# Kernel tuning notes

Measured on AMD Instinct MI355X. Metric: run time of the kernel, lower is better.

The kernel has to match this reference:

```python
import jax, jax.numpy as jnp
import numpy as np

B, T, F, U, O = 256, 1024, 37, 64, 1


def setup_inputs() -> dict:
    key = jax.random.key(0)
    ks = jax.random.split(key, 8)
    return {
        "demo": jax.random.normal(ks[0], (B, 8), dtype=jnp.float32),
        "times": jax.random.uniform(ks[1], (B, T), dtype=jnp.float32),
        "values": jax.random.normal(ks[2], (B, T, F), dtype=jnp.float32),
        "measurements": jax.random.uniform(ks[3], (B, T, F), dtype=jnp.float32),
        "lengths": jax.random.randint(ks[4], (B,), 1, T + 1),
        # Keras GRU params (reset_after=True): kernel [F,3U], recurrent_kernel [U,3U], bias [2,3U]
        "kernel": jax.random.normal(ks[5], (F, 3 * U), dtype=jnp.float32) * 0.05,
        "recurrent_kernel": jax.random.normal(ks[6], (U, 3 * U), dtype=jnp.float32) * 0.05,
        "bias": jnp.zeros((2, 3 * U), dtype=jnp.float32),
        "dense_w": jax.random.normal(ks[7], (U, O), dtype=jnp.float32) * 0.05,
        "dense_b": jnp.zeros((O,), dtype=jnp.float32),
    }


def _gru_model(values, lengths, kernel, recurrent_kernel, bias, dense_w, dense_b, seq_len):
    # tf.sequence_mask(lengths, maxlen=T)
    mask = jnp.arange(seq_len)[None, :] < lengths[:, None]  # [B, T] bool
    # input projection hoisted out of the recurrence: [B, T, 3U]
    x_proj = values @ kernel + bias[0]

    n_units = recurrent_kernel.shape[0]

    def step(h, inp):
        xp, m = inp                       # xp: [B, 3U], m: [B]
        hp = h @ recurrent_kernel + bias[1]
        xz, xr, xh = jnp.split(xp, 3, axis=-1)
        hz, hr, hh = jnp.split(hp, 3, axis=-1)
        z = jax.nn.sigmoid(xz + hz)
        r = jax.nn.sigmoid(xr + hr)
        cand = jnp.tanh(xh + r * hh)      # reset_after=True: reset applied after recurrent matmul
        h_new = z * h + (1.0 - z) * cand
        # Keras masking: masked steps keep previous state/output
        h = jnp.where(m[:, None], h_new, h)
        return h, h

    h0 = jnp.zeros((values.shape[0], n_units), values.dtype)
    _, hs = jax.lax.scan(step, h0, (jnp.swapaxes(x_proj, 0, 1), jnp.swapaxes(mask, 0, 1)))
    gru_out = jnp.swapaxes(hs, 0, 1)      # [B, T, U] (return_sequences=True)
    return jax.nn.sigmoid(gru_out @ dense_w + dense_b)  # Dense with sigmoid activation


def reference(demo, times, values, measurements, lengths, kernel, recurrent_kernel, bias, dense_w, dense_b):
    # demo and measurements are accepted by call() but unused; times only supplies maxlen
    return _gru_model(values, lengths, kernel, recurrent_kernel, bias, dense_w, dense_b, times.shape[1])
```

## Files before the change

### kernel.cpp

```cpp
#include <hip/hip_runtime.h>
#include <hip/hip_fp16.h>

#define BQ 256
#define TQ 1024
#define FQ 37
#define UQ 64
#define G3 192
#define CH 8
#define NCK (TQ / CH)
#define CFD (CH * FQ)

typedef _Float16 h2v __attribute__((ext_vector_type(2)));

__device__ __forceinline__ float sigmoid_f(float x) {
    return 1.0f / (1.0f + __expf(-x));
}
__device__ __forceinline__ float tanh_f(float x) {
    return 1.0f - 2.0f / (__expf(2.0f * x) + 1.0f);
}
__device__ __forceinline__ float fdot2f(h2v a, h2v b, float c) {
#if __has_builtin(__builtin_amdgcn_fdot2)
    return __builtin_amdgcn_fdot2(a, b, c, false);
#else
    float d;
    asm("v_dot2_f32_f16 %0, %1, %2, %3" : "=v"(d) : "v"(a), "v"(b), "v"(c));
    return d;
#endif
}

__global__ __launch_bounds__(128)
__attribute__((amdgpu_waves_per_eu(1, 1)))
void gru_fused(const float* __restrict__ values,
               const int*   __restrict__ lengths,
               const float* __restrict__ Wk,
               const float* __restrict__ Wr,
               const float* __restrict__ bias,
               const float* __restrict__ dw,
               const float* __restrict__ db,
               float*       __restrict__ out)
{
    const int tid = threadIdx.x;
    const int j   = tid & 63;
    const int w   = tid >> 6;
    const int b   = blockIdx.x;

    __shared__ __align__(16) float    s_v[2][CH][40];
    __shared__ __align__(16) float4   s_xp4[2][CH][64];
    __shared__ __align__(16) _Float16 s_h16[2][CH][72];

    const float* vbp = values + (size_t)b * TQ * FQ;
    float* ob = out + (size_t)b * TQ;

    if (w == 0) {
        h2v Pz[32], Pr[32], Ph[32];
#pragma unroll
        for (int i = 0; i < 32; ++i) {
            h2v tz, tr, th;
            tz.x = (_Float16)Wr[(2 * i) * G3 + j];
            tz.y = (_Float16)Wr[(2 * i + 1) * G3 + j];
            tr.x = (_Float16)Wr[(2 * i) * G3 + 64 + j];
            tr.y = (_Float16)Wr[(2 * i + 1) * G3 + 64 + j];
            th.x = (_Float16)Wr[(2 * i) * G3 + 128 + j];
            th.y = (_Float16)Wr[(2 * i + 1) * G3 + 128 + j];
            Pz[i] = tz; Pr[i] = tr; Ph[i] = th;
        }
        const float bh  = bias[G3 + 128 + j];
        const int   len = lengths[b];

        s_h16[1][CH - 1][j] = (_Float16)0.0f;
        asm volatile("s_waitcnt lgkmcnt(0)" ::: "memory");
        __builtin_amdgcn_s_barrier();

        float h = 0.0f;
        const _Float16* prow = &s_h16[1][CH - 1][0];

#define CONSH(QI, QV)                                                         \
        {                                                                     \
            const h2v* hv = (const h2v*)&(QV);                                \
            az0 = fdot2f(Pz[4 * (QI) + 0], hv[0], az0);                       \
            az1 = fdot2f(Pz[4 * (QI) + 1], hv[1], az1);                       \
            ar0 = fdot2f(Pr[4 * (QI) + 0], hv[0], ar0);                       \
            ar1 = fdot2f(Pr[4 * (QI) + 1], hv[1], ar1);                       \
            ah0 = fdot2f(Ph[4 * (QI) + 0], hv[0], ah0);                       \
            ah1 = fdot2f(Ph[4 * (QI) + 1], hv[1], ah1);                       \
            az0 = fdot2f(Pz[4 * (QI) + 2], hv[2], az0);                       \
            az1 = fdot2f(Pz[4 * (QI) + 3], hv[3], az1);                       \
            ar0 = fdot2f(Pr[4 * (QI) + 2], hv[2], ar0);                       \
            ar1 = fdot2f(Pr[4 * (QI) + 3], hv[3], ar1);                       \
            ah0 = fdot2f(Ph[4 * (QI) + 2], hv[2], ah0);                       \
            ah1 = fdot2f(Ph[4 * (QI) + 3], hv[3], ah1);                       \
        }

#define CSTEP(TC, XQ)                                                         \
        {                                                                     \
            const float4* hp4 = (const float4*)prow;                          \
            float4 q0 = hp4[0], q1 = hp4[1], q2 = hp4[2], q3 = hp4[3],        \
                   q4 = hp4[4], q5 = hp4[5], q6 = hp4[6], q7 = hp4[7];        \
            float az0 = 0.f, az1 = 0.f, ar0 = 0.f, ar1 = 0.f,                 \
                  ah0 = 0.f, ah1 = 0.f;                                       \
            CONSH(0, q0) CONSH(1, q1) CONSH(2, q2) CONSH(3, q3)               \
            CONSH(4, q4) CONSH(5, q5) CONSH(6, q6) CONSH(7, q7)               \
            const float z  = sigmoid_f((XQ).x + (az0 + az1));                 \
            const float r  = sigmoid_f((XQ).y + (ar0 + ar1));                 \
            const float cc = tanh_f((XQ).z + r * (bh + (ah0 + ah1)));         \
            const float hn = z * h + (1.0f - z) * cc;                         \
            h = ((tbase + (TC)) < len) ? hn : h;                              \
            s_h16[pb][TC][j] = (_Float16)h;                                   \
            __builtin_amdgcn_sched_barrier(0);    \
            prow = &s_h16[pb][TC][0];                                         \
        }

#pragma unroll 1
        for (int k = 0; k < NCK; ++k) {
            const int pb = k & 1;
            const int tbase = k * CH;
            const float4* xpr = &s_xp4[pb][0][j];
            float4 xq0 = xpr[0 * 64], xq1 = xpr[1 * 64];
            float4 xq2 = xpr[2 * 64], xq3 = xpr[3 * 64];
            float4 xq4 = xpr[4 * 64], xq5 = xpr[5 * 64];
            float4 xq6 = xpr[6 * 64], xq7 = xpr[7 * 64];
            CSTEP(0, xq0) CSTEP(1, xq1) CSTEP(2, xq2) CSTEP(3, xq3)
            CSTEP(4, xq4) CSTEP(5, xq5) CSTEP(6, xq6) CSTEP(7, xq7)
            asm volatile("s_waitcnt lgkmcnt(0)" ::: "memory");
            __builtin_amdgcn_s_barrier();
        }
#undef CSTEP
#undef CONSH
    } else {
        float Kz[FQ], Kr[FQ], Kh[FQ];
#pragma unroll
        for (int f = 0; f < FQ; ++f) {
            Kz[f] = Wk[f * G3 + j];
            Kr[f] = Wk[f * G3 + 64 + j];
            Kh[f] = Wk[f * G3 + 128 + j];
        }
        const float bz  = bias[j] + bias[G3 + j];
        const float br  = bias[64 + j] + bias[G3 + 64 + j];
        const float bhx = bias[128 + j];
        const float dbv = db[0];
        float dwv[8];
#pragma unroll
        for (int i = 0; i < 8; ++i) dwv[i] = dw[(j & 7) * 8 + i];

        int rq[5], cq[5];
        bool act[5];
        float stg[5];
#pragma unroll
        for (int q = 0; q < 5; ++q) {
            const int idx = j + 64 * q;
            act[q] = idx < CFD;
            rq[q] = idx / FQ;
            cq[q] = idx - rq[q] * FQ;
            stg[q] = 0.0f;
        }

#define STAGE_LOAD(CK)                                                        \
        _Pragma("unroll")                                                     \
        for (int q = 0; q < 5; ++q)                                           \
            if (act[q]) stg[q] = vbp[(size_t)(CK) * CFD + j + 64 * q];
#define STAGE_WRITE(SB)                                                       \
        _Pragma("unroll")                                                     \
        for (int q = 0; q < 5; ++q)                                           \
            if (act[q]) s_v[SB][rq[q]][cq[q]] = stg[q];

#define XF(VAL, I) { az += (VAL) * Kz[I]; ar += (VAL) * Kr[I]; ah += (VAL) * Kh[I]; }
#define XPROW(BB)                                                             \
    _Pragma("unroll 1")                                                       \
    for (int row = 0; row < CH; ++row) {                                      \
        const float4* vr = (const float4*)&s_v[BB][row][0];                   \
        float az = bz, ar = br, ah = bhx;                                     \
        { float4 v0 = vr[0], v1 = vr[1], v2 = vr[2];                          \
          XF(v0.x, 0)  XF(v0.y, 1)  XF(v0.z, 2)  XF(v0.w, 3)                  \
          XF(v1.x, 4)  XF(v1.y, 5)  XF(v1.z, 6)  XF(v1.w, 7)                  \
          XF(v2.x, 8)  XF(v2.y, 9)  XF(v2.z, 10) XF(v2.w, 11) }               \
        { float4 v3 = vr[3], v4 = vr[4], v5 = vr[5];                          \
          XF(v3.x, 12) XF(v3.y, 13) XF(v3.z, 14) XF(v3.w, 15)                 \
          XF(v4.x, 16) XF(v4.y, 17) XF(v4.z, 18) XF(v4.w, 19)                 \
          XF(v5.x, 20) XF(v5.y, 21) XF(v5.z, 22) XF(v5.w, 23) }               \
        { float4 v6 = vr[6], v7 = vr[7], v8 = vr[8];                          \
          float f36 = s_v[BB][row][36];                                       \
          XF(v6.x, 24) XF(v6.y, 25) XF(v6.z, 26) XF(v6.w, 27)                 \
          XF(v7.x, 28) XF(v7.y, 29) XF(v7.z, 30) XF(v7.w, 31)                 \
          XF(v8.x, 32) XF(v8.y, 33) XF(v8.z, 34) XF(v8.w, 35)                 \
          XF(f36, 36) }                                                       \
        float4 xo; xo.x = az; xo.y = ar; xo.z = ah; xo.w = 0.f;               \
        s_xp4[BB][row][j] = xo;                                               \
    }

#define HEAD(HB, TB)                                                          \
    {                                                                         \
        const int e = j & 7, s = j >> 3;                                      \
        float4 hw = *(const float4*)&s_h16[HB][s][e * 8];                     \
        const h2v* hp_ = (const h2v*)&hw;                                     \
        float pp = (float)hp_[0].x * dwv[0] + (float)hp_[0].y * dwv[1]        \
                 + (float)hp_[1].x * dwv[2] + (float)hp_[1].y * dwv[3]        \
                 + (float)hp_[2].x * dwv[4] + (float)hp_[2].y * dwv[5]        \
                 + (float)hp_[3].x * dwv[6] + (float)hp_[3].y * dwv[7];       \
        pp += __shfl_xor(pp, 1, 64);                                          \
        pp += __shfl_xor(pp, 2, 64);                                          \
        pp += __shfl_xor(pp, 4, 64);                                          \
        if (e == 0) ob[(TB) + s] = sigmoid_f(pp + dbv);                       \
    }

        STAGE_LOAD(0)
        asm volatile("s_waitcnt vmcnt(0)" ::: "memory");
        STAGE_WRITE(0)
        STAGE_LOAD(1)
        asm volatile("s_waitcnt vmcnt(0)" ::: "memory");
        STAGE_WRITE(1)
        STAGE_LOAD(2)
        asm volatile("s_waitcnt lgkmcnt(0)" ::: "memory");
        XPROW(0)
        asm volatile("s_waitcnt lgkmcnt(0)" ::: "memory");
        __builtin_amdgcn_s_barrier();

#pragma unroll 1
        for (int k = 0; k < NCK; ++k) {
            const int pb = k & 1, nb = pb ^ 1;
            if (k > 0) HEAD(nb, (k - 1) * CH)
            if (k + 2 < NCK) {
                asm volatile("s_waitcnt vmcnt(0)" ::: "memory");
                STAGE_WRITE(pb)
                if (k + 3 < NCK) STAGE_LOAD(k + 3)
            }
            if (k + 1 < NCK) XPROW(nb)
            asm volatile("s_waitcnt lgkmcnt(0)" ::: "memory");
            __builtin_amdgcn_s_barrier();
        }
        HEAD((NCK - 1) & 1, (NCK - 1) * CH)

#undef STAGE_LOAD
#undef STAGE_WRITE
#undef XF
#undef XPROW
#undef HEAD
    }
}

extern "C" void kernel_launch(void* const* d_in, const int* in_sizes, int n_in,
                              void* d_out, int out_size, void* d_ws, size_t ws_size,
                              hipStream_t stream) {
    const float* values  = (const float*)d_in[2];
    const int*   lengths = (const int*)  d_in[4];
    const float* Wk      = (const float*)d_in[5];
    const float* Wr      = (const float*)d_in[6];
    const float* bias    = (const float*)d_in[7];
    const float* dw      = (const float*)d_in[8];
    const float* db      = (const float*)d_in[9];
    float* out = (float*)d_out;

    gru_fused<<<dim3(BQ), dim3(128), 0, stream>>>(
        values, lengths, Wk, Wr, bias, dw, db, out);
}
```

Before: 381.0 us.

## Broadcast hidden state via DPP and ds_bpermute instead of LDS round trip

The recurrent wave no longer reads the previous hidden state back from shared memory each step. It packs neighbouring fp16 lanes with a DPP swap, then gathers all 32 packed pairs across the wave using ds_bpermute. This is meant to remove the LDS store-then-load dependency on the serial critical path. The trade is 32 bpermute ops per step in place of 8 wide LDS reads, which may add latency. The shared-memory store is kept for the output wave.

```diff
diff --git a/kernel.cpp b/kernel.cpp
--- a/kernel.cpp
+++ b/kernel.cpp
@@ -26,6 +26,9 @@
     asm("v_dot2_f32_f16 %0, %1, %2, %3" : "=v"(d) : "v"(a), "v"(b), "v"(c));
     return d;
 #endif
+}
+__device__ __forceinline__ h2v u2h(unsigned int u) {
+    union { unsigned int x; h2v h; } v; v.x = u; return v.h;
 }
 
 __global__ __launch_bounds__(128)
@@ -67,47 +70,41 @@
         const float bh  = bias[G3 + 128 + j];
         const int   len = lengths[b];
 
-        s_h16[1][CH - 1][j] = (_Float16)0.0f;
-        asm volatile("s_waitcnt lgkmcnt(0)" ::: "memory");
         __builtin_amdgcn_s_barrier();
 
         float h = 0.0f;
-        const _Float16* prow = &s_h16[1][CH - 1][0];
-
-#define CONSH(QI, QV)                                                         \
-        {                                                                     \
-            const h2v* hv = (const h2v*)&(QV);                                \
-            az0 = fdot2f(Pz[4 * (QI) + 0], hv[0], az0);                       \
-            az1 = fdot2f(Pz[4 * (QI) + 1], hv[1], az1);                       \
-            ar0 = fdot2f(Pr[4 * (QI) + 0], hv[0], ar0);                       \
-            ar1 = fdot2f(Pr[4 * (QI) + 1], hv[1], ar1);                       \
-            ah0 = fdot2f(Ph[4 * (QI) + 0], hv[0], ah0);                       \
-            ah1 = fdot2f(Ph[4 * (QI) + 1], hv[1], ah1);                       \
-            az0 = fdot2f(Pz[4 * (QI) + 2], hv[2], az0);                       \
-            az1 = fdot2f(Pz[4 * (QI) + 3], hv[3], az1);                       \
-            ar0 = fdot2f(Pr[4 * (QI) + 2], hv[2], ar0);                       \
-            ar1 = fdot2f(Pr[4 * (QI) + 3], hv[3], ar1);                       \
-            ah0 = fdot2f(Ph[4 * (QI) + 2], hv[2], ah0);                       \
-            ah1 = fdot2f(Ph[4 * (QI) + 3], hv[3], ah1);                       \
-        }
+        int hpk = 0;
 
 #define CSTEP(TC, XQ)                                                         \
         {                                                                     \
-            const float4* hp4 = (const float4*)prow;                          \
-            float4 q0 = hp4[0], q1 = hp4[1], q2 = hp4[2], q3 = hp4[3],        \
-                   q4 = hp4[4], q5 = hp4[5], q6 = hp4[6], q7 = hp4[7];        \
+            int hv_i[32];                                                     \
+            _Pragma("unroll")                                                 \
+            for (int p = 0; p < 32; ++p)                                      \
+                hv_i[p] = __builtin_amdgcn_ds_bpermute(8 * p, hpk);           \
             float az0 = 0.f, az1 = 0.f, ar0 = 0.f, ar1 = 0.f,                 \
                   ah0 = 0.f, ah1 = 0.f;                                       \
-            CONSH(0, q0) CONSH(1, q1) CONSH(2, q2) CONSH(3, q3)               \
-            CONSH(4, q4) CONSH(5, q5) CONSH(6, q6) CONSH(7, q7)               \
+            _Pragma("unroll")                                                 \
+            for (int p = 0; p < 32; p += 2) {                                 \
+                const h2v a = u2h((unsigned int)hv_i[p]);                     \
+                const h2v c = u2h((unsigned int)hv_i[p + 1]);                 \
+                az0 = fdot2f(Pz[p],     a, az0);                              \
+                az1 = fdot2f(Pz[p + 1], c, az1);                              \
+                ar0 = fdot2f(Pr[p],     a, ar0);                              \
+                ar1 = fdot2f(Pr[p + 1], c, ar1);                              \
+                ah0 = fdot2f(Ph[p],     a, ah0);                              \
+                ah1 = fdot2f(Ph[p + 1], c, ah1);                              \
+            }                                                                 \
             const float z  = sigmoid_f((XQ).x + (az0 + az1));                 \
             const float r  = sigmoid_f((XQ).y + (ar0 + ar1));                 \
             const float cc = tanh_f((XQ).z + r * (bh + (ah0 + ah1)));         \
             const float hn = z * h + (1.0f - z) * cc;                         \
             h = ((tbase + (TC)) < len) ? hn : h;                              \
-            s_h16[pb][TC][j] = (_Float16)h;                                   \
-            __builtin_amdgcn_sched_barrier(0);    \
-            prow = &s_h16[pb][TC][0];                                         \
+            const unsigned int h16 =                                          \
+                (unsigned int)__half_as_ushort(__float2half(h));     \
+            s_h16[pb][TC][j] = *(const _Float16*)&h16;         \
+            const unsigned int nb16 = (unsigned int)__builtin_amdgcn_mov_dpp( \
+                (int)h16, 0xB1, 0xF, 0xF, true);     \
+            hpk = (int)((nb16 << 16) | (h16 & 0xFFFFu));                      \
         }
 
 #pragma unroll 1
@@ -125,7 +122,6 @@
             __builtin_amdgcn_s_barrier();
         }
 #undef CSTEP
-#undef CONSH
     } else {
         float Kz[FQ], Kr[FQ], Kh[FQ];
 #pragma unroll
```

Result: slower. 389.0 us (+2.1%).
